# Optimization experiments

Hardware: AMD Instinct MI355X
Metric: run time of the kernel (lower is better)

## Reference

```python
import jax, jax.numpy as jnp
import numpy as np

FEAT_STRIDE = 16
PRE_NMS_TOP_N = 4000   # cfg[cfg_key].RPN_PRE_NMS_TOP_N
POST_NMS_TOP_N = 300   # cfg[cfg_key].RPN_POST_NMS_TOP_N
NMS_THRESH = 0.7       # cfg[cfg_key].RPN_NMS_THRESH


def _generate_anchors(base_size=16, ratios=(0.5, 1.0, 2.0), scales=(8, 16, 32)):
    ratios = np.array(ratios, dtype=np.float64)
    scales = np.array(scales, dtype=np.float64)
    base = np.array([1, 1, base_size, base_size], dtype=np.float64) - 1

    def whctrs(a):
        w = a[2] - a[0] + 1
        h = a[3] - a[1] + 1
        return w, h, a[0] + 0.5 * (w - 1), a[1] + 0.5 * (h - 1)

    def mk(ws, hs, xc, yc):
        ws = np.atleast_1d(ws)[:, None]
        hs = np.atleast_1d(hs)[:, None]
        return np.hstack((xc - 0.5 * (ws - 1), yc - 0.5 * (hs - 1),
                          xc + 0.5 * (ws - 1), yc + 0.5 * (hs - 1)))

    w, h, xc, yc = whctrs(base)
    size = w * h
    ws = np.round(np.sqrt(size / ratios))
    hs = np.round(ws * ratios)
    ratio_anchors = mk(ws, hs, xc, yc)
    out = []
    for i in range(ratio_anchors.shape[0]):
        w, h, xc, yc = whctrs(ratio_anchors[i])
        out.append(mk(w * scales, h * scales, xc, yc))
    return np.vstack(out).astype(np.float32)  # [9,4]


def _nms_keep(boxes, thresh):
    # boxes sorted by score desc, [N,4]; torchvision-style IoU (no +1).
    x1, y1, x2, y2 = boxes[:, 0], boxes[:, 1], boxes[:, 2], boxes[:, 3]
    areas = (x2 - x1) * (y2 - y1)
    lt = jnp.maximum(boxes[:, None, :2], boxes[None, :, :2])
    rb = jnp.minimum(boxes[:, None, 2:], boxes[None, :, 2:])
    wh = jnp.clip(rb - lt, 0.0)
    inter = wh[..., 0] * wh[..., 1]
    iou = inter / (areas[:, None] + areas[None, :] - inter + 1e-9)  # [N,N]
    N = boxes.shape[0]
    idx = jnp.arange(N)
    def body(i, keep):
        sup = (iou[i] > thresh) & (idx > i) & keep[i]
        return keep & ~sup
    return jax.lax.fori_loop(0, N, body, jnp.ones((N,), jnp.bool_))


def _per_image(boxes, scores):
    # pre-NMS top-k by score (matches sort-desc + slice)
    _, order = jax.lax.top_k(scores, PRE_NMS_TOP_N)
    b = boxes[order]
    keep = _nms_keep(jax.lax.stop_gradient(b), NMS_THRESH)
    rank = jnp.cumsum(keep) - 1                       # position among kept
    tgt = jnp.where(keep, rank, POST_NMS_TOP_N)       # OOB indices are dropped
    return jnp.zeros((POST_NMS_TOP_N, 4), boxes.dtype).at[tgt].set(b, mode='drop')


def reference(scores, bbox_deltas, im_info, anchors):
    B, A, H, W = scores.shape
    # anchor shifts over the feature grid
    sx = jnp.arange(W, dtype=scores.dtype) * FEAT_STRIDE
    sy = jnp.arange(H, dtype=scores.dtype) * FEAT_STRIDE
    yy, xx = jnp.meshgrid(sy, sx, indexing='ij')
    shifts = jnp.stack([xx.ravel(), yy.ravel(), xx.ravel(), yy.ravel()], axis=1)  # [K,4]
    all_anchors = (anchors[None, :, :] + shifts[:, None, :]).reshape(-1, 4)       # [K*A,4]

    deltas = bbox_deltas.transpose(0, 2, 3, 1).reshape(B, -1, 4)  # [B,K*A,4]
    sc = scores.transpose(0, 2, 3, 1).reshape(B, -1)              # [B,K*A]

    # bbox_transform_inv
    w = all_anchors[:, 2] - all_anchors[:, 0] + 1.0
    h = all_anchors[:, 3] - all_anchors[:, 1] + 1.0
    cx = all_anchors[:, 0] + 0.5 * w
    cy = all_anchors[:, 1] + 0.5 * h
    pcx = deltas[..., 0] * w + cx
    pcy = deltas[..., 1] * h + cy
    pw = jnp.exp(deltas[..., 2]) * w
    ph = jnp.exp(deltas[..., 3]) * h
    props = jnp.stack([pcx - 0.5 * pw, pcy - 0.5 * ph,
                       pcx + 0.5 * pw, pcy + 0.5 * ph], axis=-1)  # [B,K*A,4]

    # clip_boxes: x in [0, im_w-1], y in [0, im_h-1]
    hi = jnp.stack([im_info[:, 1] - 1, im_info[:, 0] - 1,
                    im_info[:, 1] - 1, im_info[:, 0] - 1], axis=1)  # [B,4]
    props = jnp.clip(props, 0.0, hi[:, None, :])

    boxes_out = jax.vmap(_per_image)(props, sc)  # [B,POST,4]
    batch_col = jnp.broadcast_to(
        jnp.arange(B, dtype=scores.dtype)[:, None, None], (B, POST_NMS_TOP_N, 1))
    return jnp.concatenate([batch_col, boxes_out], axis=-1)  # [B,POST,5]


def setup_inputs():
    key = jax.random.key(0)
    k1, k2 = jax.random.split(key)
    B, A, H, W = 4, 9, 50, 76
    scores = jax.random.normal(k1, (B, A, H, W), jnp.float32)
    bbox_deltas = jax.random.normal(k2, (B, 4 * A, H, W), jnp.float32) * 0.2
    im_info = jnp.tile(jnp.array([[800.0, 1216.0, 1.0]], jnp.float32), (B, 1))
    anchors = jnp.asarray(_generate_anchors())
    return {"scores": scores, "bbox_deltas": bbox_deltas,
            "im_info": im_info, "anchors": anchors}
```

## Files before the change

kernel.cpp:

```cpp
#include <hip/hip_runtime.h>
#include <stdint.h>

#define A_N 9
#define H_N 50
#define W_N 76
#define HW_N (H_N * W_N)
#define N_PROP (A_N * HW_N)
#define B_N 4
#define PRE_NMS 4000
#define POST_NMS 300
#define NMS_TH 0.7f
#define SORT_N 4096
#define MASK_WORDS 64
#define CAND_MAX 5120
#define NBINS 4096
#define NPAIR 32
#define NLW 5
#define DEC_BLKS ((N_PROP + 255) / 256)

__global__ __launch_bounds__(256) void decode_kernel(
    const float* __restrict__ scores,
    const float* __restrict__ deltas,
    const float* __restrict__ im_info,
    const float* __restrict__ anchors,
    float4* __restrict__ boxes,
    unsigned long long* __restrict__ keys,
    unsigned* __restrict__ ghist) {
#pragma clang fp contract(off)
    __shared__ unsigned hist[NBINS];
    int tid = threadIdx.x;
    int b = blockIdx.y;
    int r = blockIdx.x * 256 + tid;
#pragma unroll
    for (int i = 0; i < NBINS / 256; ++i) hist[tid + i * 256] = 0u;
    __syncthreads();

    if (r < N_PROP) {
        int a = r / HW_N;
        int hw = r - a * HW_N;
        int hy = hw / W_N;
        int wx = hw - hy * W_N;

        float sx = (float)wx * 16.0f;
        float sy = (float)hy * 16.0f;
        float ax1 = anchors[a * 4 + 0] + sx;
        float ay1 = anchors[a * 4 + 1] + sy;
        float ax2 = anchors[a * 4 + 2] + sx;
        float ay2 = anchors[a * 4 + 3] + sy;
        float aw = ax2 - ax1 + 1.0f;
        float ah = ay2 - ay1 + 1.0f;
        float cx = ax1 + 0.5f * aw;
        float cy = ay1 + 0.5f * ah;

        const float* db = deltas + ((size_t)b * 36 + (size_t)a * 4) * HW_N + hw;
        float d0 = db[0];
        float d1 = db[HW_N];
        float d2 = db[2 * HW_N];
        float d3 = db[3 * HW_N];

        float pcx = d0 * aw + cx;
        float pcy = d1 * ah + cy;
        float pw  = expf(d2) * aw;
        float ph  = expf(d3) * ah;

        float x1 = pcx - 0.5f * pw;
        float y1 = pcy - 0.5f * ph;
        float x2 = pcx + 0.5f * pw;
        float y2 = pcy + 0.5f * ph;

        float xhi = im_info[b * 3 + 1] - 1.0f;
        float yhi = im_info[b * 3 + 0] - 1.0f;
        x1 = fminf(fmaxf(x1, 0.0f), xhi);
        y1 = fminf(fmaxf(y1, 0.0f), yhi);
        x2 = fminf(fmaxf(x2, 0.0f), xhi);
        y2 = fminf(fmaxf(y2, 0.0f), yhi);

        boxes[(size_t)b * N_PROP + r] = make_float4(x1, y1, x2, y2);

        float s = scores[((size_t)b * A_N + a) * HW_N + hw];
        unsigned f = __float_as_uint(s);
        unsigned sk = f ^ ((f & 0x80000000u) ? 0xFFFFFFFFu : 0x80000000u);
        unsigned n_ref = (unsigned)(hw * A_N + a);
        unsigned long long key = ((unsigned long long)sk << 32) | (unsigned)(~n_ref);
        keys[(size_t)b * N_PROP + r] = key;
        atomicAdd(&hist[(unsigned)(key >> 52)], 1u);
    }
    __syncthreads();
#pragma unroll
    for (int i = 0; i < NBINS / 256; ++i) {
        unsigned v = hist[tid + i * 256];
        if (v) atomicAdd(&ghist[b * NBINS + tid + i * 256], v);
    }
}

__global__ __launch_bounds__(64) void findT_kernel(const unsigned* __restrict__ ghist,
                                                   int* __restrict__ Tout) {
    __shared__ unsigned h[NBINS];
    int b = blockIdx.x;
    int lane = threadIdx.x;
    for (int i = lane; i < NBINS; i += 64) h[i] = ghist[b * NBINS + i];
    __syncthreads();
    unsigned gsum = 0;
    for (int j = 0; j < 64; ++j) gsum += h[lane * 64 + j];
    unsigned s = gsum;
    for (int d = 1; d < 64; d <<= 1) {
        unsigned t = (unsigned)__shfl_down((int)s, d);
        if (lane + d < 64) s += t;
    }
    unsigned long long bal = __ballot(s >= PRE_NMS);
    int gstar = 63 - __builtin_clzll(bal);
    unsigned after = (gstar < 63) ? (unsigned)__builtin_amdgcn_readlane((int)s, gstar + 1) : 0u;
    unsigned R = PRE_NMS - after;
    unsigned s2 = h[gstar * 64 + lane];
    for (int d = 1; d < 64; d <<= 1) {
        unsigned t = (unsigned)__shfl_down((int)s2, d);
        if (lane + d < 64) s2 += t;
    }
    unsigned long long bal2 = __ballot(s2 >= R);
    int j = 63 - __builtin_clzll(bal2);
    if (lane == 0) Tout[b] = gstar * 64 + j;
}

__global__ void compact_kernel(const unsigned long long* __restrict__ keys,
                               const int* __restrict__ T,
                               unsigned* __restrict__ cnt,
                               unsigned long long* __restrict__ cand) {
    int b = blockIdx.y;
    int n = blockIdx.x * 256 + threadIdx.x;
    bool pred = false;
    unsigned long long k = 0ull;
    if (n < N_PROP) {
        k = keys[(size_t)b * N_PROP + n];
        pred = ((int)(unsigned)(k >> 52) >= T[b]);
    }
    unsigned long long m = __ballot(pred);
    if (m) {
        int lane = threadIdx.x & 63;
        int lead = __ffsll((unsigned long long)m) - 1;
        unsigned base = 0;
        if (lane == lead) base = atomicAdd(&cnt[b], (unsigned)__popcll(m));
        base = __shfl((int)base, lead);
        if (pred) {
            unsigned pos = base + (unsigned)__popcll(m & ((1ull << lane) - 1ull));
            if (pos < CAND_MAX) cand[(size_t)b * CAND_MAX + pos] = k;
        }
    }
}

__global__ __launch_bounds__(256) void rank_scatter_kernel(
    const unsigned long long* __restrict__ cand,
    const unsigned* __restrict__ cnt,
    const float4* __restrict__ boxes,
    float4* __restrict__ sortedBoxes) {
    __shared__ unsigned long long sk[256];
    int b = blockIdx.y;
    int tid = threadIdx.x;
    int ci = blockIdx.x * 64 + (tid >> 2);
    int q = tid & 3;
    int mc = (int)min(cnt[b], (unsigned)CAND_MAX);
    unsigned long long my = (ci < mc) ? cand[(size_t)b * CAND_MAX + ci] : 0ull;
    int rank = 0;
    int nt = (mc + 255) >> 8;
    for (int t = 0; t < nt; ++t) {
        int j = t * 256 + tid;
        sk[tid] = (j < mc) ? cand[(size_t)b * CAND_MAX + j] : 0ull;
        __syncthreads();
#pragma unroll 16
        for (int c = 0; c < 64; ++c) {
            int cc = q * 64 + ((c + q * 17) & 63);
            rank += (sk[cc] > my) ? 1 : 0;
        }
        __syncthreads();
    }
    rank += __shfl_xor(rank, 1);
    rank += __shfl_xor(rank, 2);
    if (q == 0 && ci < mc && rank < PRE_NMS) {
        unsigned n_ref = ~(unsigned)(my & 0xFFFFFFFFull);
        unsigned a = n_ref % A_N;
        unsigned hw = n_ref / A_N;
        sortedBoxes[(size_t)b * SORT_N + rank] =
            boxes[(size_t)b * N_PROP + a * HW_N + hw];
    }
    if (q == 1) {
        int pi = blockIdx.x * 64 + (tid >> 2);
        if (pi >= PRE_NMS && pi < SORT_N)
            sortedBoxes[(size_t)b * SORT_N + pi] = make_float4(0.f, 0.f, 0.f, 0.f);
    }
}

__global__ __launch_bounds__(256) void iou_mask_kernel(
    const float4* __restrict__ sortedBoxes,
    unsigned long long* __restrict__ colmaj,
    unsigned long long* __restrict__ rowmaj) {
#pragma clang fp contract(off)
    int b = blockIdx.y;
    int wv = threadIdx.x >> 6;
    int t = threadIdx.x & 63;
    int k = blockIdx.x * 4 + wv;
    int rc = 0;
    while (k >= 64 - rc) { k -= 64 - rc; ++rc; }
    int cc = rc + k;

    __shared__ float4 colb[4][64];
    colb[wv][t] = sortedBoxes[(size_t)b * SORT_N + cc * 64 + t];
    __syncthreads();

    int r = rc * 64 + t;
    float4 rb = sortedBoxes[(size_t)b * SORT_N + r];
    float rarea = (rb.z - rb.x) * (rb.w - rb.y);
    unsigned long long word = 0ull;
    for (int c = 0; c < 64; ++c) {
        int j = cc * 64 + c;
        float4 cb = colb[wv][c];
        float carea = (cb.z - cb.x) * (cb.w - cb.y);
        float ltx = fmaxf(rb.x, cb.x);
        float lty = fmaxf(rb.y, cb.y);
        float rbx = fminf(rb.z, cb.z);
        float rby = fminf(rb.w, cb.w);
        float iw = fmaxf(rbx - ltx, 0.0f);
        float ih = fmaxf(rby - lty, 0.0f);
        float inter = iw * ih;
        float iou = inter / (rarea + carea - inter + 1e-9f);
        if (iou > NMS_TH && j > r) word |= (1ull << c);
    }
    colmaj[((size_t)b * MASK_WORDS + cc) * SORT_N + r] = word;
    rowmaj[((size_t)b * SORT_N + r) * MASK_WORDS + cc] = word;
}

__device__ __forceinline__ unsigned long long rl64(unsigned long long v, int src) {
    unsigned lo = (unsigned)__builtin_amdgcn_readlane((int)(unsigned)(v & 0xFFFFFFFFull), src);
    unsigned hi = (unsigned)__builtin_amdgcn_readlane((int)(unsigned)(v >> 32), src);
    return ((unsigned long long)hi << 32) | lo;
}

__device__ __forceinline__ unsigned long long redor64(unsigned long long alive,
                                                      unsigned long long v, int lane) {
    unsigned long long x = ((alive >> lane) & 1ull) ? v : 0ull;
    x |= __shfl_xor(x, 1);
    x |= __shfl_xor(x, 2);
    x |= __shfl_xor(x, 4);
    x |= __shfl_xor(x, 8);
    x |= __shfl_xor(x, 16);
    x |= __shfl_xor(x, 32);
    return x;
}

__device__ __forceinline__ void block_sync() {
    asm volatile("s_waitcnt lgkmcnt(0)" ::: "memory");
    __builtin_amdgcn_s_barrier();
    asm volatile("" ::: "memory");
}

#define GLOAD(dst, addr) \
    asm volatile("global_load_dwordx2 %0, %1, off" : "=v"(dst) : "v"(addr))
#define WAITV0 asm volatile("s_waitcnt vmcnt(0)" ::: "memory")
#define SCHED0 __builtin_amdgcn_sched_barrier(0)

#define TILE_COL(P, t) ((t) < 6 ? 2 * (P) + (t) : 2 * (P) + 1 + ((t) - 6))
#define TILE_RB(P, t)  ((size_t)((t) < 6 ? 2 * (P) : 2 * (P) + 1) << 6)
#define TILE_ADDR(P, t) \
    (C + (size_t)(TILE_COL(P, t) < 64 ? TILE_COL(P, t) : 63) * SORT_N + TILE_RB(P, t) + lane)

#define ISSUE_PAIR(P)                                                          \
    do {                                                                       \
        pf_vmask = 0u;                                                         \
        GLOAD(pf0,  TILE_ADDR(P, 0));  if (TILE_COL(P, 0)  < 64) pf_vmask |= 1u << 0;  \
        GLOAD(pf1,  TILE_ADDR(P, 1));  if (TILE_COL(P, 1)  < 64) pf_vmask |= 1u << 1;  \
        GLOAD(pf2,  TILE_ADDR(P, 2));  if (TILE_COL(P, 2)  < 64) pf_vmask |= 1u << 2;  \
        GLOAD(pf3,  TILE_ADDR(P, 3));  if (TILE_COL(P, 3)  < 64) pf_vmask |= 1u << 3;  \
        GLOAD(pf4,  TILE_ADDR(P, 4));  if (TILE_COL(P, 4)  < 64) pf_vmask |= 1u << 4;  \
        GLOAD(pf5,  TILE_ADDR(P, 5));  if (TILE_COL(P, 5)  < 64) pf_vmask |= 1u << 5;  \
        GLOAD(pf6,  TILE_ADDR(P, 6));  if (TILE_COL(P, 6)  < 64) pf_vmask |= 1u << 6;  \
        GLOAD(pf7,  TILE_ADDR(P, 7));  if (TILE_COL(P, 7)  < 64) pf_vmask |= 1u << 7;  \
        GLOAD(pf8,  TILE_ADDR(P, 8));  if (TILE_COL(P, 8)  < 64) pf_vmask |= 1u << 8;  \
        GLOAD(pf9,  TILE_ADDR(P, 9));  if (TILE_COL(P, 9)  < 64) pf_vmask |= 1u << 9;  \
        GLOAD(pf10, TILE_ADDR(P, 10)); if (TILE_COL(P, 10) < 64) pf_vmask |= 1u << 10; \
    } while (0)

#define NEXTROW2(rk)                                                           \
    int rk;                                                                    \
    {                                                                          \
        if (xA) { int bb_ = __builtin_ctzll(xA); xA &= xA - 1; rk = baseA + bb_; } \
        else if (xB) { int bb_ = __builtin_ctzll(xB); xB &= xB - 1; rk = baseB + bb_; } \
        else rk = rpad;                                                        \
    }

__global__ __launch_bounds__(512, 1) void nms_scan_kernel(
    const unsigned long long* __restrict__ colmaj,
    const unsigned long long* __restrict__ rowmaj,
    const float4* __restrict__ sortedBoxes,
    float* __restrict__ out) {
    int b = blockIdx.x;
    int tid = threadIdx.x;
    int lane = tid & 63;
    int wv = tid >> 6;
    const unsigned long long* C = colmaj + (size_t)b * MASK_WORDS * SORT_N;
    const unsigned long long* R = rowmaj + (size_t)b * SORT_N * MASK_WORDS;

    __shared__ int kept[POST_NMS];
    __shared__ unsigned remW[MASK_WORDS][2];
    __shared__ unsigned long long aliveLds[MASK_WORDS];
    __shared__ unsigned long long ring[4][11][64];
    __shared__ unsigned long long car2[2][2];
    __shared__ int doneLds;
    __shared__ int kcntLds;

    if (tid < MASK_WORDS) { remW[tid][0] = 0u; remW[tid][1] = 0u; aliveLds[tid] = 0ull; }
    if (tid < 4) car2[tid >> 1][tid & 1] = 0ull;
    if (tid == 0) { doneLds = 0; kcntLds = 0; }

    unsigned long long pf0=0,pf1=0,pf2=0,pf3=0,pf4=0,pf5=0,pf6=0,pf7=0,pf8=0,pf9=0,pf10=0;
    unsigned pf_vmask = 0u;
    bool pf_have = false;
    unsigned long long gp0=0,gp1=0,gp2=0,gp3=0,gp4=0,gp5=0,gp6=0,gp7=0;
    bool ld_valid = false;

    if (wv == 1) {
        for (int t = 0; t < 11; ++t) {
            int col = TILE_COL(0, t);
            unsigned long long v =
                (col < 64) ? C[(size_t)col * SORT_N + TILE_RB(0, t) + lane] : 0ull;
            ring[0][t][lane] = v;
        }
        ISSUE_PAIR(1);
        pf_have = true;
    }
    block_sync();

    unsigned long long carA = 0ull, carB = 0ull;
    int kcnt = 0;

    for (int q = 0; q < NPAIR; ++q) {
        if (wv == 0) {
            int A = 2 * q, Bg = A + 1, slot = q & 3;
            unsigned long long dA  = ring[slot][0][lane];
            unsigned long long tA1 = ring[slot][1][lane];
            unsigned long long tA2 = ring[slot][2][lane];
            unsigned long long tA3 = ring[slot][3][lane];
            unsigned long long dB  = ring[slot][6][lane];
            unsigned long long tB1 = ring[slot][7][lane];
            unsigned long long tB2 = ring[slot][8][lane];
            unsigned long long remA =
                ((unsigned long long)remW[A][1] << 32) | (unsigned long long)remW[A][0];
            unsigned long long remB =
                ((unsigned long long)remW[Bg][1] << 32) | (unsigned long long)remW[Bg][0];
            unsigned long long h2A = car2[q & 1][0];
            unsigned long long h2B = car2[q & 1][1];
            bool hit = false;
            unsigned long long aliveA = 0ull, aliveB = 0ull;
            unsigned long long pend = ~(remA | carA | h2A);
            while (pend) {
                int bit = __builtin_ctzll(pend);
                if (lane == 0) kept[kcnt] = (A << 6) + bit;
                ++kcnt;
                aliveA |= 1ull << bit;
                if (kcnt == POST_NMS) { hit = true; break; }
                pend &= ~(rl64(dA, bit) | (1ull << bit));
            }
            if (!hit) {
                unsigned long long nA1 = redor64(aliveA, tA1, lane);
                pend = ~(remB | carB | h2B | nA1);
                while (pend) {
                    int bit = __builtin_ctzll(pend);
                    if (lane == 0) kept[kcnt] = (Bg << 6) + bit;
                    ++kcnt;
                    aliveB |= 1ull << bit;
                    if (kcnt == POST_NMS) { hit = true; break; }
                    pend &= ~(rl64(dB, bit) | (1ull << bit));
                }
            }
            carA = redor64(aliveA, tA2, lane) | redor64(aliveB, tB1, lane);
            carB = redor64(aliveA, tA3, lane) | redor64(aliveB, tB2, lane);
            if (lane == 0) {
                aliveLds[A]  = aliveA;
                aliveLds[Bg] = aliveB;
                kcntLds = kcnt;
                if (hit) doneLds = 1;
            }
        } else if (wv == 1) {
            if (pf_have) {
                WAITV0;
                SCHED0;
                int wp = q + 1;
                if (wp < NPAIR) {
                    int ws = wp & 3;
                    ring[ws][0][lane]  = (pf_vmask & (1u << 0))  ? pf0  : 0ull;
                    ring[ws][1][lane]  = (pf_vmask & (1u << 1))  ? pf1  : 0ull;
                    ring[ws][2][lane]  = (pf_vmask & (1u << 2))  ? pf2  : 0ull;
                    ring[ws][3][lane]  = (pf_vmask & (1u << 3))  ? pf3  : 0ull;
                    ring[ws][4][lane]  = (pf_vmask & (1u << 4))  ? pf4  : 0ull;
                    ring[ws][5][lane]  = (pf_vmask & (1u << 5))  ? pf5  : 0ull;
                    ring[ws][6][lane]  = (pf_vmask & (1u << 6))  ? pf6  : 0ull;
                    ring[ws][7][lane]  = (pf_vmask & (1u << 7))  ? pf7  : 0ull;
                    ring[ws][8][lane]  = (pf_vmask & (1u << 8))  ? pf8  : 0ull;
                    ring[ws][9][lane]  = (pf_vmask & (1u << 9))  ? pf9  : 0ull;
                    ring[ws][10][lane] = (pf_vmask & (1u << 10)) ? pf10 : 0ull;
                }
                pf_have = false;
            }
            int ip = q + 2;
            if (ip < NPAIR) {
                ISSUE_PAIR(ip);
                pf_have = true;
            }
        } else if (wv == 2) {
            if (q >= 1) {
                int p = q - 1, sp = p & 3;
                unsigned long long aA = aliveLds[2 * p];
                unsigned long long aB = aliveLds[2 * p + 1];
                unsigned long long tA4 = ring[sp][4][lane];
                unsigned long long tA5 = ring[sp][5][lane];
                unsigned long long tB3 = ring[sp][9][lane];
                unsigned long long tB4 = ring[sp][10][lane];
                unsigned long long c0 = redor64(aA, tA4, lane) | redor64(aB, tB3, lane);
                unsigned long long c1 = redor64(aA, tA5, lane) | redor64(aB, tB4, lane);
                if (lane == 0) {
                    car2[(q + 1) & 1][0] = c0;
                    car2[(q + 1) & 1][1] = c1;
                }
            }
        } else {
            if (ld_valid) {
                WAITV0;
                SCHED0;
                unsigned long long acc =
                    ((gp0 | gp1) | (gp2 | gp3)) | ((gp4 | gp5) | (gp6 | gp7));
                unsigned lo = (unsigned)acc, hi = (unsigned)(acc >> 32);
                if (lo) atomicOr(&remW[lane][0], lo);
                if (hi) atomicOr(&remW[lane][1], hi);
                ld_valid = false;
            }
            if (q >= 1) {
                int p = q - 1, gA = 2 * p, gB = 2 * p + 1;
                unsigned long long aA = aliveLds[gA];
                unsigned long long aB = aliveLds[gB];
                int k = wv - 3;
                unsigned long long below = (1ull << lane) - 1ull;
                bool inA = (aA >> lane) & 1ull;
                bool inB = (aB >> lane) & 1ull;
                int posA = (int)__popcll(aA & below);
                int posB = (int)__popcll(aA) + (int)__popcll(aB & below);
                unsigned long long mA = __ballot(inA && (posA % NLW) == k);
                unsigned long long mB = __ballot(inB && (posB % NLW) == k);
                if (mA | mB) {
                    int baseA = gA << 6, baseB = gB << 6;
                    unsigned long long xA = mA, xB = mB;
                    int rpad = mA ? (baseA + __builtin_ctzll(mA))
                                  : (baseB + __builtin_ctzll(mB));
                    NEXTROW2(r0) NEXTROW2(r1) NEXTROW2(r2) NEXTROW2(r3)
                    NEXTROW2(r4) NEXTROW2(r5) NEXTROW2(r6) NEXTROW2(r7)
                    const unsigned long long* Rb = R + lane;
                    GLOAD(gp0, Rb + (size_t)r0 * MASK_WORDS);
                    GLOAD(gp1, Rb + (size_t)r1 * MASK_WORDS);
                    GLOAD(gp2, Rb + (size_t)r2 * MASK_WORDS);
                    GLOAD(gp3, Rb + (size_t)r3 * MASK_WORDS);
                    GLOAD(gp4, Rb + (size_t)r4 * MASK_WORDS);
                    GLOAD(gp5, Rb + (size_t)r5 * MASK_WORDS);
                    GLOAD(gp6, Rb + (size_t)r6 * MASK_WORDS);
                    GLOAD(gp7, Rb + (size_t)r7 * MASK_WORDS);
                    ld_valid = true;
                    unsigned long long ovf = 0ull;
                    while (xA) {
                        int bb = __builtin_ctzll(xA); xA &= xA - 1;
                        ovf |= Rb[(size_t)(baseA + bb) * MASK_WORDS];
                    }
                    while (xB) {
                        int bb = __builtin_ctzll(xB); xB &= xB - 1;
                        ovf |= Rb[(size_t)(baseB + bb) * MASK_WORDS];
                    }
                    if (ovf) {
                        unsigned lo = (unsigned)ovf, hi = (unsigned)(ovf >> 32);
                        if (lo) atomicOr(&remW[lane][0], lo);
                        if (hi) atomicOr(&remW[lane][1], hi);
                    }
                }
            }
        }
        block_sync();
        if (doneLds) break;
    }

    WAITV0;
    __syncthreads();

    int kc = kcntLds;
    for (int r = tid; r < POST_NMS; r += 512) {
        float* o = out + ((size_t)b * POST_NMS + r) * 5;
        float4 bx = make_float4(0.f, 0.f, 0.f, 0.f);
        if (r < kc) bx = sortedBoxes[(size_t)b * SORT_N + kept[r]];
        o[0] = (float)b;
        o[1] = bx.x;
        o[2] = bx.y;
        o[3] = bx.z;
        o[4] = bx.w;
    }
}

extern "C" void kernel_launch(void* const* d_in, const int* in_sizes, int n_in,
                              void* d_out, int out_size, void* d_ws, size_t ws_size,
                              hipStream_t stream) {
    const float* scores  = (const float*)d_in[0];
    const float* deltas  = (const float*)d_in[1];
    const float* im_info = (const float*)d_in[2];
    const float* anchors = (const float*)d_in[3];
    float* out = (float*)d_out;

    char* ws = (char*)d_ws;
    size_t off = 0;
    float4* boxes = (float4*)(ws + off);
    off += (size_t)B_N * N_PROP * sizeof(float4);
    off = (off + 255) & ~(size_t)255;
    unsigned long long* keys = (unsigned long long*)(ws + off);
    off += (size_t)B_N * N_PROP * sizeof(unsigned long long);
    off = (off + 255) & ~(size_t)255;
    float4* sortedBoxes = (float4*)(ws + off);
    off += (size_t)B_N * SORT_N * sizeof(float4);
    off = (off + 255) & ~(size_t)255;
    unsigned long long* colmaj = (unsigned long long*)(ws + off);
    off += (size_t)B_N * MASK_WORDS * SORT_N * sizeof(unsigned long long);
    off = (off + 255) & ~(size_t)255;
    unsigned long long* rowmaj = (unsigned long long*)(ws + off);
    off += (size_t)B_N * SORT_N * MASK_WORDS * sizeof(unsigned long long);
    off = (off + 255) & ~(size_t)255;
    unsigned long long* cand = (unsigned long long*)(ws + off);
    off += (size_t)B_N * CAND_MAX * sizeof(unsigned long long);
    off = (off + 255) & ~(size_t)255;
    unsigned* ghist = (unsigned*)(ws + off);
    size_t zero_off = off;
    off += (size_t)B_N * NBINS * sizeof(unsigned);
    unsigned* cnt = (unsigned*)(ws + off);
    off += (size_t)B_N * sizeof(unsigned);
    size_t zero_bytes = off - zero_off;
    off = (off + 255) & ~(size_t)255;
    int* Tbuf = (int*)(ws + off);
    off += (size_t)B_N * sizeof(int);

    hipMemsetAsync((void*)ghist, 0, zero_bytes, stream);

    decode_kernel<<<dim3(DEC_BLKS, B_N), 256, 0, stream>>>(
        scores, deltas, im_info, anchors, boxes, keys, ghist);
    findT_kernel<<<B_N, 64, 0, stream>>>(ghist, Tbuf);
    compact_kernel<<<dim3((N_PROP + 255) / 256, B_N), 256, 0, stream>>>(
        keys, Tbuf, cnt, cand);
    rank_scatter_kernel<<<dim3(CAND_MAX / 64, B_N), 256, 0, stream>>>(
        cand, cnt, boxes, sortedBoxes);
    iou_mask_kernel<<<dim3(520, B_N), 256, 0, stream>>>(sortedBoxes, colmaj, rowmaj);
    nms_scan_kernel<<<B_N, 512, 0, stream>>>(colmaj, rowmaj, sortedBoxes, out);
}
```

Before: 214.5 us.

## Fuse decode, threshold search and compaction into one per-image kernel

Merges the decode, histogram threshold search and candidate compaction kernels, plus the memset, into a single kernel with one 1024-thread block per image. The histogram and candidate counter now live in shared memory, which removes the global atomics and three launch boundaries. In exchange, each image is processed by one block (four blocks in total), so most of the GPU sits idle during the roughly 34k-element decode per image.

```diff
diff --git a/kernel.cpp b/kernel.cpp
--- a/kernel.cpp
+++ b/kernel.cpp
@@ -16,135 +16,132 @@
 #define NBINS 4096
 #define NPAIR 32
 #define NLW 5
-#define DEC_BLKS ((N_PROP + 255) / 256)
-
-__global__ __launch_bounds__(256) void decode_kernel(
+
+__global__ __launch_bounds__(1024) void front_kernel(
     const float* __restrict__ scores,
     const float* __restrict__ deltas,
     const float* __restrict__ im_info,
     const float* __restrict__ anchors,
     float4* __restrict__ boxes,
     unsigned long long* __restrict__ keys,
-    unsigned* __restrict__ ghist) {
+    unsigned* __restrict__ cnt,
+    unsigned long long* __restrict__ cand) {
 #pragma clang fp contract(off)
     __shared__ unsigned hist[NBINS];
-    int tid = threadIdx.x;
-    int b = blockIdx.y;
-    int r = blockIdx.x * 256 + tid;
-#pragma unroll
-    for (int i = 0; i < NBINS / 256; ++i) hist[tid + i * 256] = 0u;
+    __shared__ int Tlds;
+    __shared__ unsigned cntL;
+    const int b = blockIdx.x;
+    const int tid = threadIdx.x;
+
+    for (int i = tid; i < NBINS; i += 1024) hist[i] = 0u;
+    if (tid == 0) cntL = 0u;
     __syncthreads();
 
-    if (r < N_PROP) {
-        int a = r / HW_N;
-        int hw = r - a * HW_N;
-        int hy = hw / W_N;
-        int wx = hw - hy * W_N;
-
-        float sx = (float)wx * 16.0f;
-        float sy = (float)hy * 16.0f;
-        float ax1 = anchors[a * 4 + 0] + sx;
-        float ay1 = anchors[a * 4 + 1] + sy;
-        float ax2 = anchors[a * 4 + 2] + sx;
-        float ay2 = anchors[a * 4 + 3] + sy;
-        float aw = ax2 - ax1 + 1.0f;
-        float ah = ay2 - ay1 + 1.0f;
-        float cx = ax1 + 0.5f * aw;
-        float cy = ay1 + 0.5f * ah;
-
-        const float* db = deltas + ((size_t)b * 36 + (size_t)a * 4) * HW_N + hw;
-        float d0 = db[0];
-        float d1 = db[HW_N];
-        float d2 = db[2 * HW_N];
-        float d3 = db[3 * HW_N];
-
-        float pcx = d0 * aw + cx;
-        float pcy = d1 * ah + cy;
-        float pw  = expf(d2) * aw;
-        float ph  = expf(d3) * ah;
-
-        float x1 = pcx - 0.5f * pw;
-        float y1 = pcy - 0.5f * ph;
-        float x2 = pcx + 0.5f * pw;
-        float y2 = pcy + 0.5f * ph;
-
-        float xhi = im_info[b * 3 + 1] - 1.0f;
-        float yhi = im_info[b * 3 + 0] - 1.0f;
-        x1 = fminf(fmaxf(x1, 0.0f), xhi);
-        y1 = fminf(fmaxf(y1, 0.0f), yhi);
-        x2 = fminf(fmaxf(x2, 0.0f), xhi);
-        y2 = fminf(fmaxf(y2, 0.0f), yhi);
-
-        boxes[(size_t)b * N_PROP + r] = make_float4(x1, y1, x2, y2);
-
-        float s = scores[((size_t)b * A_N + a) * HW_N + hw];
-        unsigned f = __float_as_uint(s);
-        unsigned sk = f ^ ((f & 0x80000000u) ? 0xFFFFFFFFu : 0x80000000u);
-        unsigned n_ref = (unsigned)(hw * A_N + a);
-        unsigned long long key = ((unsigned long long)sk << 32) | (unsigned)(~n_ref);
-        keys[(size_t)b * N_PROP + r] = key;
-        atomicAdd(&hist[(unsigned)(key >> 52)], 1u);
+    const float xhi = im_info[b * 3 + 1] - 1.0f;
+    const float yhi = im_info[b * 3 + 0] - 1.0f;
+    for (int it = 0; it < (N_PROP + 1023) / 1024; ++it) {
+        int r = it * 1024 + tid;
+        if (r < N_PROP) {
+            int a = r / HW_N;
+            int hw = r - a * HW_N;
+            int hy = hw / W_N;
+            int wx = hw - hy * W_N;
+
+            float sx = (float)wx * 16.0f;
+            float sy = (float)hy * 16.0f;
+            float ax1 = anchors[a * 4 + 0] + sx;
+            float ay1 = anchors[a * 4 + 1] + sy;
+            float ax2 = anchors[a * 4 + 2] + sx;
+            float ay2 = anchors[a * 4 + 3] + sy;
+            float aw = ax2 - ax1 + 1.0f;
+            float ah = ay2 - ay1 + 1.0f;
+            float cx = ax1 + 0.5f * aw;
+            float cy = ay1 + 0.5f * ah;
+
+            const float* db = deltas + ((size_t)b * 36 + (size_t)a * 4) * HW_N + hw;
+            float d0 = db[0];
+            float d1 = db[HW_N];
+            float d2 = db[2 * HW_N];
+            float d3 = db[3 * HW_N];
+
+            float pcx = d0 * aw + cx;
+            float pcy = d1 * ah + cy;
+            float pw  = expf(d2) * aw;
+            float ph  = expf(d3) * ah;
+
+            float x1 = pcx - 0.5f * pw;
+            float y1 = pcy - 0.5f * ph;
+            float x2 = pcx + 0.5f * pw;
+            float y2 = pcy + 0.5f * ph;
+
+            x1 = fminf(fmaxf(x1, 0.0f), xhi);
+            y1 = fminf(fmaxf(y1, 0.0f), yhi);
+            x2 = fminf(fmaxf(x2, 0.0f), xhi);
+            y2 = fminf(fmaxf(y2, 0.0f), yhi);
+
+            boxes[(size_t)b * N_PROP + r] = make_float4(x1, y1, x2, y2);
+
+            float s = scores[((size_t)b * A_N + a) * HW_N + hw];
+            unsigned f = __float_as_uint(s);
+            unsigned sk = f ^ ((f & 0x80000000u) ? 0xFFFFFFFFu : 0x80000000u);
+            unsigned n_ref = (unsigned)(hw * A_N + a);
+            unsigned long long key =
+                ((unsigned long long)sk << 32) | (unsigned)(~n_ref);
+            keys[(size_t)b * N_PROP + r] = key;
+            atomicAdd(&hist[(unsigned)(key >> 52)], 1u);
+        }
     }
     __syncthreads();
-#pragma unroll
-    for (int i = 0; i < NBINS / 256; ++i) {
-        unsigned v = hist[tid + i * 256];
-        if (v) atomicAdd(&ghist[b * NBINS + tid + i * 256], v);
-    }
-}
-
-__global__ __launch_bounds__(64) void findT_kernel(const unsigned* __restrict__ ghist,
-                                                   int* __restrict__ Tout) {
-    __shared__ unsigned h[NBINS];
-    int b = blockIdx.x;
-    int lane = threadIdx.x;
-    for (int i = lane; i < NBINS; i += 64) h[i] = ghist[b * NBINS + i];
+
+    if (tid < 64) {
+        int lane = tid;
+        unsigned gsum = 0;
+        for (int j = 0; j < 64; ++j) gsum += hist[lane * 64 + j];
+        unsigned s = gsum;
+        for (int d = 1; d < 64; d <<= 1) {
+            unsigned t = (unsigned)__shfl_down((int)s, d);
+            if (lane + d < 64) s += t;
+        }
+        unsigned long long bal = __ballot(s >= PRE_NMS);
+        int gstar = 63 - __builtin_clzll(bal);
+        unsigned after = (gstar < 63)
+            ? (unsigned)__builtin_amdgcn_readlane((int)s, gstar + 1) : 0u;
+        unsigned R = PRE_NMS - after;
+        unsigned s2 = hist[gstar * 64 + lane];
+        for (int d = 1; d < 64; d <<= 1) {
+            unsigned t = (unsigned)__shfl_down((int)s2, d);
+            if (lane + d < 64) s2 += t;
+        }
+        unsigned long long bal2 = __ballot(s2 >= R);
+        int j = 63 - __builtin_clzll(bal2);
+        if (lane == 0) Tlds = gstar * 64 + j;
+    }
     __syncthreads();
-    unsigned gsum = 0;
-    for (int j = 0; j < 64; ++j) gsum += h[lane * 64 + j];
-    unsigned s = gsum;
-    for (int d = 1; d < 64; d <<= 1) {
-        unsigned t = (unsigned)__shfl_down((int)s, d);
-        if (lane + d < 64) s += t;
-    }
-    unsigned long long bal = __ballot(s >= PRE_NMS);
-    int gstar = 63 - __builtin_clzll(bal);
-    unsigned after = (gstar < 63) ? (unsigned)__builtin_amdgcn_readlane((int)s, gstar + 1) : 0u;
-    unsigned R = PRE_NMS - after;
-    unsigned s2 = h[gstar * 64 + lane];
-    for (int d = 1; d < 64; d <<= 1) {
-        unsigned t = (unsigned)__shfl_down((int)s2, d);
-        if (lane + d < 64) s2 += t;
-    }
-    unsigned long long bal2 = __ballot(s2 >= R);
-    int j = 63 - __builtin_clzll(bal2);
-    if (lane == 0) Tout[b] = gstar * 64 + j;
-}
-
-__global__ void compact_kernel(const unsigned long long* __restrict__ keys,
-                               const int* __restrict__ T,
-                               unsigned* __restrict__ cnt,
-                               unsigned long long* __restrict__ cand) {
-    int b = blockIdx.y;
-    int n = blockIdx.x * 256 + threadIdx.x;
-    bool pred = false;
-    unsigned long long k = 0ull;
-    if (n < N_PROP) {
-        k = keys[(size_t)b * N_PROP + n];
-        pred = ((int)(unsigned)(k >> 52) >= T[b]);
-    }
-    unsigned long long m = __ballot(pred);
-    if (m) {
-        int lane = threadIdx.x & 63;
-        int lead = __ffsll((unsigned long long)m) - 1;
-        unsigned base = 0;
-        if (lane == lead) base = atomicAdd(&cnt[b], (unsigned)__popcll(m));
-        base = __shfl((int)base, lead);
-        if (pred) {
-            unsigned pos = base + (unsigned)__popcll(m & ((1ull << lane) - 1ull));
-            if (pos < CAND_MAX) cand[(size_t)b * CAND_MAX + pos] = k;
-        }
-    }
+
+    const int Tb = Tlds;
+    for (int it = 0; it < (N_PROP + 1023) / 1024; ++it) {
+        int n = it * 1024 + tid;
+        bool pred = false;
+        unsigned long long k = 0ull;
+        if (n < N_PROP) {
+            k = keys[(size_t)b * N_PROP + n];
+            pred = ((int)(unsigned)(k >> 52) >= Tb);
+        }
+        unsigned long long m = __ballot(pred);
+        if (m) {
+            int lane = tid & 63;
+            int lead = __ffsll((unsigned long long)m) - 1;
+            unsigned base = 0;
+            if (lane == lead) base = atomicAdd(&cntL, (unsigned)__popcll(m));
+            base = __shfl((int)base, lead);
+            if (pred) {
+                unsigned pos = base + (unsigned)__popcll(m & ((1ull << lane) - 1ull));
+                if (pos < CAND_MAX) cand[(size_t)b * CAND_MAX + pos] = k;
+            }
+        }
+    }
+    __syncthreads();
+    if (tid == 0) cnt[b] = cntL;
 }
 
 __global__ __launch_bounds__(256) void rank_scatter_kernel(
@@ -525,23 +522,11 @@
     unsigned long long* cand = (unsigned long long*)(ws + off);
     off += (size_t)B_N * CAND_MAX * sizeof(unsigned long long);
     off = (off + 255) & ~(size_t)255;
-    unsigned* ghist = (unsigned*)(ws + off);
-    size_t zero_off = off;
-    off += (size_t)B_N * NBINS * sizeof(unsigned);
     unsigned* cnt = (unsigned*)(ws + off);
     off += (size_t)B_N * sizeof(unsigned);
-    size_t zero_bytes = off - zero_off;
-    off = (off + 255) & ~(size_t)255;
-    int* Tbuf = (int*)(ws + off);
-    off += (size_t)B_N * sizeof(int);
-
-    hipMemsetAsync((void*)ghist, 0, zero_bytes, stream);
-
-    decode_kernel<<<dim3(DEC_BLKS, B_N), 256, 0, stream>>>(
-        scores, deltas, im_info, anchors, boxes, keys, ghist);
-    findT_kernel<<<B_N, 64, 0, stream>>>(ghist, Tbuf);
-    compact_kernel<<<dim3((N_PROP + 255) / 256, B_N), 256, 0, stream>>>(
-        keys, Tbuf, cnt, cand);
+
+    front_kernel<<<B_N, 1024, 0, stream>>>(
+        scores, deltas, im_info, anchors, boxes, keys, cnt, cand);
     rank_scatter_kernel<<<dim3(CAND_MAX / 64, B_N), 256, 0, stream>>>(
         cand, cnt, boxes, sortedBoxes);
     iou_mask_kernel<<<dim3(520, B_N), 256, 0, stream>>>(sortedBoxes, colmaj, rowmaj);
```

After: 219.9 us. +2.5%, slower.
